# Kernel tuning notes

Hardware: AMD Instinct MI355X
Metric: run time of the kernel (lower is better)

The kernel has to match this reference:

```python
import jax, jax.numpy as jnp
import numpy as np

B, S, F, DK = 8, 2048, 1024, 128

def setup_inputs() -> dict:
    key = jax.random.key(0)
    ks = jax.random.split(key, 6)
    scale = 0.02
    return {
        "q": jax.random.normal(ks[0], (B, S, F), dtype=jnp.float32),
        "k": jax.random.normal(ks[1], (B, S, F), dtype=jnp.float32),
        "v": jax.random.normal(ks[2], (B, S, F), dtype=jnp.float32),
        "w_q": jax.random.normal(ks[3], (F, DK), dtype=jnp.float32) * scale,
        "w_k": jax.random.normal(ks[4], (F, DK), dtype=jnp.float32) * scale,
        "w_v": jax.random.normal(ks[5], (F, DK), dtype=jnp.float32) * scale,
    }

def reference(q, k, v, w_q, w_k, w_v):
    d_k = w_q.shape[-1]
    # bias-free linear projections: [B,S,F] @ [F,DK] -> [B,S,DK]
    qp = jnp.einsum("bsf,fd->bsd", q, w_q)
    kp = jnp.einsum("bsf,fd->bsd", k, w_k)
    vp = jnp.einsum("bsf,fd->bsd", v, w_v)
    # scaled dot-product scores: [B,S,S]
    scores = jnp.einsum("bqd,bkd->bqk", qp, kp) * (1.0 / jnp.sqrt(jnp.float32(d_k)))
    attn = jax.nn.softmax(scores, axis=-1)
    out = jnp.einsum("bqk,bkd->bqd", attn, vp)
    return out
```

## Files before the change

### kernel.cpp

```cpp
#include <hip/hip_runtime.h>
#include <hip/hip_bf16.h>

#define B_ 8
#define S_ 2048
#define F_ 1024
#define DK_ 128
#define M_ (B_*S_)

typedef unsigned short u16;
typedef short short8 __attribute__((ext_vector_type(8)));
typedef float f32x4 __attribute__((ext_vector_type(4)));
typedef float f32x16 __attribute__((ext_vector_type(16)));

__device__ __forceinline__ u16 f2bf(float f) {
    unsigned int u = __float_as_uint(f);
    u += 0x7FFFu + ((u >> 16) & 1u);
    return (u16)(u >> 16);
}
__device__ __forceinline__ unsigned int pack2(float a, float b) {
    return (unsigned int)f2bf(a) | ((unsigned int)f2bf(b) << 16);
}
__device__ __forceinline__ float fexp2(float x) {
#if __has_builtin(__builtin_amdgcn_exp2f)
    return __builtin_amdgcn_exp2f(x);
#else
    return exp2f(x);
#endif
}
__device__ __forceinline__ unsigned int cvt_pk_bf16(float lo, float hi) {
    unsigned int r;
    asm volatile("v_cvt_pk_bf16_f32 %0, %1, %2" : "=v"(r) : "v"(lo), "v"(hi));
    return r;
}

__global__ __launch_bounds__(256) void prep_wt(const float* __restrict__ wq,
                                               const float* __restrict__ wk,
                                               const float* __restrict__ wv,
                                               u16* __restrict__ WT) {
    int id = blockIdx.x * 256 + threadIdx.x;
    if (id >= 3 * DK_ * F_) return;
    int m   = id / (DK_ * F_);
    int rem = id - m * (DK_ * F_);
    int c   = rem / F_;
    int k   = rem - c * F_;
    const float* w = (m == 0) ? wq : (m == 1) ? wk : wv;
    float v = w[k * DK_ + c];
    if (m == 0) v *= 0.12751741951f;
    WT[id] = f2bf(v);
}

__global__ __launch_bounds__(256, 3) void proj(const float* __restrict__ xq,
                                               const float* __restrict__ xk,
                                               const float* __restrict__ xv,
                                               const u16* __restrict__ WT,
                                               u16* __restrict__ qp,
                                               u16* __restrict__ kp,
                                               u16* __restrict__ vpT) {
    const int mode = blockIdx.y;
    const float* X = (mode == 0) ? xq : (mode == 1) ? xk : xv;
    const u16*   W = WT + mode * (DK_ * F_);

    __shared__ u16 a_lds[64][40];
    __shared__ u16 w_lds[128][40];

    const int t    = threadIdx.x;
    const int lane = t & 63;
    const int wv_  = t >> 6;
    const int l15  = lane & 15, l4 = lane >> 4;
    const int row0 = blockIdx.x * 64;

    f32x4 acc[8];
#pragma unroll
    for (int j = 0; j < 8; ++j) acc[j] = f32x4{0.f, 0.f, 0.f, 0.f};

    for (int k0 = 0; k0 < F_; k0 += 32) {
        {
            int r = t >> 2, kk = (t & 3) * 8;
            const float4* src = (const float4*)(X + (size_t)(row0 + r) * F_ + k0 + kk);
            float4 f0 = src[0], f1 = src[1];
            int4 o0;
            o0.x = pack2(f0.x, f0.y); o0.y = pack2(f0.z, f0.w);
            o0.z = pack2(f1.x, f1.y); o0.w = pack2(f1.z, f1.w);
            *(int4*)&a_lds[r][kk] = o0;
        }
        {
            int c = t >> 1, kk = (t & 1) * 16;
            const int4* src = (const int4*)(W + (size_t)c * F_ + k0 + kk);
            *(int4*)&w_lds[c][kk]     = src[0];
            *(int4*)&w_lds[c][kk + 8] = src[1];
        }
        __syncthreads();

        short8 af = *(const short8*)&a_lds[wv_ * 16 + l15][l4 * 8];
        short8 bf[8];
#pragma unroll
        for (int ct = 0; ct < 8; ++ct)
            bf[ct] = *(const short8*)&w_lds[ct * 16 + l15][l4 * 8];

        if (mode < 2) {
#pragma unroll
            for (int ct = 0; ct < 8; ++ct)
                acc[ct] = __builtin_amdgcn_mfma_f32_16x16x32_bf16(af, bf[ct], acc[ct], 0, 0, 0);
        } else {
#pragma unroll
            for (int ct = 0; ct < 8; ++ct)
                acc[ct] = __builtin_amdgcn_mfma_f32_16x16x32_bf16(bf[ct], af, acc[ct], 0, 0, 0);
        }
        __syncthreads();
    }

    if (mode < 2) {
        u16* OUT = (mode == 0) ? qp : kp;
#pragma unroll
        for (int ct = 0; ct < 8; ++ct)
#pragma unroll
            for (int r = 0; r < 4; ++r) {
                int row = row0 + wv_ * 16 + l4 * 4 + r;
                int col = ct * 16 + l15;
                OUT[(size_t)row * DK_ + col] = f2bf(acc[ct][r]);
            }
    } else {
#pragma unroll
        for (int ct = 0; ct < 8; ++ct)
#pragma unroll
            for (int r = 0; r < 4; ++r) {
                int n = ct * 16 + l4 * 4 + r;
                int m = row0 + wv_ * 16 + l15;
                vpT[(size_t)n * M_ + m] = f2bf(acc[ct][r]);
            }
    }
}

union attn_lds_t {
    struct {
        __align__(16) unsigned char kbuf[2][16384];
        __align__(16) unsigned char vbuf[2][16384];
    } s;
    struct { float ob[64][132]; } e;
};

__global__ __launch_bounds__(512, 2) void attn(const u16* __restrict__ qp,
                                               const u16* __restrict__ kp,
                                               const u16* __restrict__ vpT,
                                               float* __restrict__ out) {
    __shared__ attn_lds_t u;
    __shared__ float m_lds[4][32], l_lds[4][32], gm_lds[2][32], gl_lds[2][32];

    const int t      = threadIdx.x;
    const int lane   = t & 63;
    const int wv_    = t >> 6;
    const int q_sub  = wv_ & 1;
    const int kv_sub = (wv_ >> 1) & 1;
    const int d_half = wv_ >> 2;
    const int r31    = lane & 31;
    const int hi     = lane >> 5;

    const int b  = blockIdx.x & 7;
    const int qi = blockIdx.x >> 3;
    const int qrow0 = b * S_ + qi * 64;
    const int kvb0  = b * S_;

    short8 qf[8];
#pragma unroll
    for (int c = 0; c < 8; ++c)
        qf[c] = *(const short8*)(qp + (size_t)(qrow0 + q_sub * 32 + r31) * DK_
                                    + c * 16 + hi * 8);

    f32x16 o4[2];
#pragma unroll
    for (int ct = 0; ct < 2; ++ct)
#pragma unroll
        for (int i = 0; i < 16; ++i) o4[ct][i] = 0.f;
    float mrun = -1.0e30f, lrun = 0.f;

    int4 gk0, gk1, gv0, gv1;
    const int f0 = t, f1 = 512 + t;
    const int kr0 = f0 >> 4, kc0 = f0 & 15, kr1 = f1 >> 4, kc1 = f1 & 15;
    const int vr0 = f0 >> 3, vc0 = f0 & 7,  vr1 = f1 >> 3, vc1 = f1 & 7;

#define LOADT(kvb)                                                               \
    {                                                                            \
        gk0 = *(const int4*)(kp + (size_t)((kvb) + kr0) * DK_ + kc0 * 8);        \
        gk1 = *(const int4*)(kp + (size_t)((kvb) + kr1) * DK_ + kc1 * 8);        \
        gv0 = *(const int4*)(vpT + (size_t)vr0 * M_ + (kvb) + vc0 * 8);          \
        gv1 = *(const int4*)(vpT + (size_t)vr1 * M_ + (kvb) + vc1 * 8);          \
    }
#define WRITET(nb)                                                               \
    {                                                                            \
        *(int4*)(u.s.kbuf[nb] + kr0 * 256 + ((kc0 ^ (kr0 & 15)) << 4)) = gk0;    \
        *(int4*)(u.s.kbuf[nb] + kr1 * 256 + ((kc1 ^ (kr1 & 15)) << 4)) = gk1;    \
        *(int4*)(u.s.vbuf[nb] + vr0 * 128 + ((vc0 ^ (vr0 & 7)) << 4)) = gv0;     \
        *(int4*)(u.s.vbuf[nb] + vr1 * 128 + ((vc1 ^ (vr1 & 7)) << 4)) = gv1;     \
    }

    LOADT(kvb0);
    WRITET(0);
    int cur = 0;

    for (int kt = 0; kt < 32; ++kt) {
        __syncthreads();

        if (kt < 31) LOADT(kvb0 + (kt + 1) * 64);

        const unsigned char* kb = u.s.kbuf[cur];
        const unsigned char* vb = u.s.vbuf[cur];

        const int krow  = kv_sub * 32 + r31;
        const int kbase = krow * 256;
        const int ksw   = krow & 15;
        short8 kf[8];
#pragma unroll
        for (int c = 0; c < 8; ++c)
            kf[c] = *(const short8*)(kb + kbase + (((c * 2 + hi) ^ ksw) << 4));

        f32x16 st;
#pragma unroll
        for (int i = 0; i < 16; ++i) st[i] = 0.f;
#pragma unroll
        for (int c = 0; c < 8; ++c)
            st = __builtin_amdgcn_mfma_f32_32x32x16_bf16(kf[c], qf[c], st, 0, 0, 0);

        float tm = st[0];
#pragma unroll
        for (int i = 1; i < 16; ++i) tm = fmaxf(tm, st[i]);
        tm = fmaxf(tm, __shfl_xor(tm, 32, 64));
        if (__any(tm > mrun + 8.0f)) {
            float mn = fmaxf(mrun, tm);
            float fs = fexp2(mrun - mn);
            mrun = mn;
            lrun *= fs;
#pragma unroll
            for (int ct = 0; ct < 2; ++ct)
#pragma unroll
                for (int i = 0; i < 16; ++i) o4[ct][i] *= fs;
        }
        float sum = 0.f;
#pragma unroll
        for (int i = 0; i < 16; ++i) { st[i] = fexp2(st[i] - mrun); sum += st[i]; }
        sum += __shfl_xor(sum, 32, 64);
        lrun += sum;

        short8 bp[2];
#pragma unroll
        for (int ch = 0; ch < 2; ++ch) {
            unsigned int wa = cvt_pk_bf16(st[ch * 8 + 0], st[ch * 8 + 1]);
            unsigned int wb = cvt_pk_bf16(st[ch * 8 + 2], st[ch * 8 + 3]);
            unsigned int wc = cvt_pk_bf16(st[ch * 8 + 4], st[ch * 8 + 5]);
            unsigned int wd = cvt_pk_bf16(st[ch * 8 + 6], st[ch * 8 + 7]);
            unsigned int xa = (unsigned int)__shfl_xor((int)wa, 32, 64);
            unsigned int xb = (unsigned int)__shfl_xor((int)wb, 32, 64);
            unsigned int xc = (unsigned int)__shfl_xor((int)wc, 32, 64);
            unsigned int xd = (unsigned int)__shfl_xor((int)wd, 32, 64);
            int4 w;
            w.x = (int)(hi ? xc : wa);
            w.y = (int)(hi ? xd : wb);
            w.z = (int)(hi ? wc : xa);
            w.w = (int)(hi ? wd : xb);
            bp[ch] = *(short8*)&w;
        }

        if (kt < 31) WRITET(cur ^ 1);

#pragma unroll
        for (int ct = 0; ct < 2; ++ct) {
            const int vrow  = d_half * 64 + ct * 32 + r31;
            const int vbase = vrow * 128;
            const int vsw   = vrow & 7;
#pragma unroll
            for (int ch = 0; ch < 2; ++ch) {
                short8 vf = *(const short8*)(vb + vbase
                                             + (((kv_sub * 4 + ch * 2 + hi) ^ vsw) << 4));
                o4[ct] = __builtin_amdgcn_mfma_f32_32x32x16_bf16(vf, bp[ch], o4[ct], 0, 0, 0);
            }
        }

        cur ^= 1;
    }
#undef LOADT
#undef WRITET

    __syncthreads();
    if (d_half == 0 && lane < 32) {
        m_lds[q_sub * 2 + kv_sub][r31] = mrun;
        l_lds[q_sub * 2 + kv_sub][r31] = lrun;
    }
    __syncthreads();
    if (t < 64) {
        int qs = t >> 5, qq = t & 31;
        float m0 = m_lds[qs * 2][qq], m1 = m_lds[qs * 2 + 1][qq];
        float gm = fmaxf(m0, m1);
        float gl = l_lds[qs * 2][qq] * fexp2(m0 - gm)
                 + l_lds[qs * 2 + 1][qq] * fexp2(m1 - gm);
        gm_lds[qs][qq] = gm;
        gl_lds[qs][qq] = gl;
    }
    __syncthreads();

    const float sc = fexp2(mrun - gm_lds[q_sub][r31]);
    const int qrow = q_sub * 32 + r31;
    if (kv_sub == 0) {
#pragma unroll
        for (int ct = 0; ct < 2; ++ct)
#pragma unroll
            for (int i = 0; i < 16; ++i) {
                int d = d_half * 64 + ct * 32 + (i & 3) + 8 * (i >> 2) + 4 * hi;
                u.e.ob[qrow][d] = o4[ct][i] * sc;
            }
    }
    __syncthreads();
    if (kv_sub == 1) {
#pragma unroll
        for (int ct = 0; ct < 2; ++ct)
#pragma unroll
            for (int i = 0; i < 16; ++i) {
                int d = d_half * 64 + ct * 32 + (i & 3) + 8 * (i >> 2) + 4 * hi;
                u.e.ob[qrow][d] += o4[ct][i] * sc;
            }
    }
    __syncthreads();

    {
        int row = t >> 3, d0 = (t & 7) * 16;
        float inv = 1.0f / gl_lds[row >> 5][row & 31];
        float* dst = out + (size_t)(qrow0 + row) * DK_ + d0;
#pragma unroll
        for (int j = 0; j < 16; j += 4) {
            float4 v;
            v.x = u.e.ob[row][d0 + j]     * inv;
            v.y = u.e.ob[row][d0 + j + 1] * inv;
            v.z = u.e.ob[row][d0 + j + 2] * inv;
            v.w = u.e.ob[row][d0 + j + 3] * inv;
            *(float4*)(dst + j) = v;
        }
    }
}

extern "C" void kernel_launch(void* const* d_in, const int* in_sizes, int n_in,
                              void* d_out, int out_size, void* d_ws, size_t ws_size,
                              hipStream_t stream) {
    const float* q  = (const float*)d_in[0];
    const float* k  = (const float*)d_in[1];
    const float* v  = (const float*)d_in[2];
    const float* wq = (const float*)d_in[3];
    const float* wk = (const float*)d_in[4];
    const float* wv = (const float*)d_in[5];
    float* out = (float*)d_out;

    char* ws = (char*)d_ws;
    u16* WT  = (u16*)ws;
    u16* qp  = (u16*)(ws + 786432);
    u16* kp  = (u16*)(ws + 786432 + 4194304);
    u16* vpT = (u16*)(ws + 786432 + 2 * 4194304);

    prep_wt<<<dim3(1536), dim3(256), 0, stream>>>(wq, wk, wv, WT);
    proj<<<dim3(256, 3), dim3(256), 0, stream>>>(q, k, v, WT, qp, kp, vpT);
    attn<<<dim3(256), dim3(512), 0, stream>>>(qp, kp, vpT, out);
}
```

Before: 83.50 us.

## Halve attention query tile to 32 rows and use permlane32 swap for P repack

The attention kernel now processes 32 query rows per block with 256 threads and launches 512 blocks instead of 256 blocks of 512 threads. The aim is to fill more CUs on the MI355X, at the cost of loading every K/V tile twice as often overall. It also splits the QK^T MFMA chain into two independent accumulators to shorten the dependency chain. The shuffle-plus-select repack of P is replaced with v_permlane32_swap, and the cross-half max and sum shuffles are deferred or folded into the final LDS reduction.

After: 85.88 us. 1.03x slower.

```diff
diff --git a/kernel.cpp b/kernel.cpp
--- a/kernel.cpp
+++ b/kernel.cpp
@@ -31,6 +31,9 @@
     unsigned int r;
     asm volatile("v_cvt_pk_bf16_f32 %0, %1, %2" : "=v"(r) : "v"(lo), "v"(hi));
     return r;
+}
+__device__ __forceinline__ void pl32_swap(unsigned int& a, unsigned int& b) {
+    asm volatile("v_permlane32_swap_b32 %0, %1" : "+v"(a), "+v"(b));
 }
 
 __global__ __launch_bounds__(256) void prep_wt(const float* __restrict__ wq,
@@ -136,35 +139,33 @@
         __align__(16) unsigned char kbuf[2][16384];
         __align__(16) unsigned char vbuf[2][16384];
     } s;
-    struct { float ob[64][132]; } e;
+    struct { float ob[32][132]; } e;
 };
 
-__global__ __launch_bounds__(512, 2) void attn(const u16* __restrict__ qp,
+__global__ __launch_bounds__(256, 2) void attn(const u16* __restrict__ qp,
                                                const u16* __restrict__ kp,
                                                const u16* __restrict__ vpT,
                                                float* __restrict__ out) {
     __shared__ attn_lds_t u;
-    __shared__ float m_lds[4][32], l_lds[4][32], gm_lds[2][32], gl_lds[2][32];
+    __shared__ float m_lds[2][32], l_lds[2][2][32], gm_lds[32], gl_lds[32];
 
     const int t      = threadIdx.x;
     const int lane   = t & 63;
     const int wv_    = t >> 6;
-    const int q_sub  = wv_ & 1;
-    const int kv_sub = (wv_ >> 1) & 1;
-    const int d_half = wv_ >> 2;
+    const int kv_sub = wv_ & 1;
+    const int d_half = wv_ >> 1;
     const int r31    = lane & 31;
     const int hi     = lane >> 5;
 
     const int b  = blockIdx.x & 7;
     const int qi = blockIdx.x >> 3;
-    const int qrow0 = b * S_ + qi * 64;
+    const int qrow0 = b * S_ + qi * 32;
     const int kvb0  = b * S_;
 
     short8 qf[8];
 #pragma unroll
     for (int c = 0; c < 8; ++c)
-        qf[c] = *(const short8*)(qp + (size_t)(qrow0 + q_sub * 32 + r31) * DK_
-                                    + c * 16 + hi * 8);
+        qf[c] = *(const short8*)(qp + (size_t)(qrow0 + r31) * DK_ + c * 16 + hi * 8);
 
     f32x16 o4[2];
 #pragma unroll
@@ -173,24 +174,30 @@
         for (int i = 0; i < 16; ++i) o4[ct][i] = 0.f;
     float mrun = -1.0e30f, lrun = 0.f;
 
-    int4 gk0, gk1, gv0, gv1;
-    const int f0 = t, f1 = 512 + t;
-    const int kr0 = f0 >> 4, kc0 = f0 & 15, kr1 = f1 >> 4, kc1 = f1 & 15;
-    const int vr0 = f0 >> 3, vc0 = f0 & 7,  vr1 = f1 >> 3, vc1 = f1 & 7;
-
-#define LOADT(kvb)                                                               \
-    {                                                                            \
-        gk0 = *(const int4*)(kp + (size_t)((kvb) + kr0) * DK_ + kc0 * 8);        \
-        gk1 = *(const int4*)(kp + (size_t)((kvb) + kr1) * DK_ + kc1 * 8);        \
-        gv0 = *(const int4*)(vpT + (size_t)vr0 * M_ + (kvb) + vc0 * 8);          \
-        gv1 = *(const int4*)(vpT + (size_t)vr1 * M_ + (kvb) + vc1 * 8);          \
-    }
-#define WRITET(nb)                                                               \
-    {                                                                            \
-        *(int4*)(u.s.kbuf[nb] + kr0 * 256 + ((kc0 ^ (kr0 & 15)) << 4)) = gk0;    \
-        *(int4*)(u.s.kbuf[nb] + kr1 * 256 + ((kc1 ^ (kr1 & 15)) << 4)) = gk1;    \
-        *(int4*)(u.s.vbuf[nb] + vr0 * 128 + ((vc0 ^ (vr0 & 7)) << 4)) = gv0;     \
-        *(int4*)(u.s.vbuf[nb] + vr1 * 128 + ((vc1 ^ (vr1 & 7)) << 4)) = gv1;     \
+    int4 gk[4], gv[4];
+    int kr[4], kc[4], vr[4], vc[4];
+#pragma unroll
+    for (int j = 0; j < 4; ++j) {
+        int f = t + 256 * j;
+        kr[j] = f >> 4; kc[j] = f & 15;
+        vr[j] = f >> 3; vc[j] = f & 7;
+    }
+
+#define LOADT(kvb)                                                                \
+    {                                                                             \
+        _Pragma("unroll")                                                         \
+        for (int j = 0; j < 4; ++j) {                                             \
+            gk[j] = *(const int4*)(kp + (size_t)((kvb) + kr[j]) * DK_ + kc[j] * 8);\
+            gv[j] = *(const int4*)(vpT + (size_t)vr[j] * M_ + (kvb) + vc[j] * 8); \
+        }                                                                         \
+    }
+#define WRITET(nb)                                                                \
+    {                                                                             \
+        _Pragma("unroll")                                                         \
+        for (int j = 0; j < 4; ++j) {                                             \
+            *(int4*)(u.s.kbuf[nb] + kr[j] * 256 + ((kc[j] ^ (kr[j] & 15)) << 4)) = gk[j]; \
+            *(int4*)(u.s.vbuf[nb] + vr[j] * 128 + ((vc[j] ^ (vr[j] & 7)) << 4)) = gv[j];  \
+        }                                                                         \
     }
 
     LOADT(kvb0);
@@ -213,18 +220,23 @@
         for (int c = 0; c < 8; ++c)
             kf[c] = *(const short8*)(kb + kbase + (((c * 2 + hi) ^ ksw) << 4));
 
+        f32x16 sa, sb;
+#pragma unroll
+        for (int i = 0; i < 16; ++i) { sa[i] = 0.f; sb[i] = 0.f; }
+#pragma unroll
+        for (int c = 0; c < 4; ++c) {
+            sa = __builtin_amdgcn_mfma_f32_32x32x16_bf16(kf[c],     qf[c],     sa, 0, 0, 0);
+            sb = __builtin_amdgcn_mfma_f32_32x32x16_bf16(kf[c + 4], qf[c + 4], sb, 0, 0, 0);
+        }
         f32x16 st;
 #pragma unroll
-        for (int i = 0; i < 16; ++i) st[i] = 0.f;
-#pragma unroll
-        for (int c = 0; c < 8; ++c)
-            st = __builtin_amdgcn_mfma_f32_32x32x16_bf16(kf[c], qf[c], st, 0, 0, 0);
+        for (int i = 0; i < 16; ++i) st[i] = sa[i] + sb[i];
 
         float tm = st[0];
 #pragma unroll
         for (int i = 1; i < 16; ++i) tm = fmaxf(tm, st[i]);
-        tm = fmaxf(tm, __shfl_xor(tm, 32, 64));
         if (__any(tm > mrun + 8.0f)) {
+            tm = fmaxf(tm, __shfl_xor(tm, 32, 64));
             float mn = fmaxf(mrun, tm);
             float fs = fexp2(mrun - mn);
             mrun = mn;
@@ -234,28 +246,26 @@
 #pragma unroll
                 for (int i = 0; i < 16; ++i) o4[ct][i] *= fs;
         }
-        float sum = 0.f;
-#pragma unroll
-        for (int i = 0; i < 16; ++i) { st[i] = fexp2(st[i] - mrun); sum += st[i]; }
-        sum += __shfl_xor(sum, 32, 64);
-        lrun += sum;
+        float s0 = 0.f, s1 = 0.f;
+#pragma unroll
+        for (int i = 0; i < 16; i += 2) {
+            st[i]     = fexp2(st[i] - mrun);
+            st[i + 1] = fexp2(st[i + 1] - mrun);
+            s0 += st[i]; s1 += st[i + 1];
+        }
+        lrun += s0 + s1;
 
         short8 bp[2];
 #pragma unroll
         for (int ch = 0; ch < 2; ++ch) {
-            unsigned int wa = cvt_pk_bf16(st[ch * 8 + 0], st[ch * 8 + 1]);
-            unsigned int wb = cvt_pk_bf16(st[ch * 8 + 2], st[ch * 8 + 3]);
-            unsigned int wc = cvt_pk_bf16(st[ch * 8 + 4], st[ch * 8 + 5]);
-            unsigned int wd = cvt_pk_bf16(st[ch * 8 + 6], st[ch * 8 + 7]);
-            unsigned int xa = (unsigned int)__shfl_xor((int)wa, 32, 64);
-            unsigned int xb = (unsigned int)__shfl_xor((int)wb, 32, 64);
-            unsigned int xc = (unsigned int)__shfl_xor((int)wc, 32, 64);
-            unsigned int xd = (unsigned int)__shfl_xor((int)wd, 32, 64);
+            unsigned int A1 = cvt_pk_bf16(st[ch * 8 + 0], st[ch * 8 + 1]);
+            unsigned int A2 = cvt_pk_bf16(st[ch * 8 + 2], st[ch * 8 + 3]);
+            unsigned int A3 = cvt_pk_bf16(st[ch * 8 + 4], st[ch * 8 + 5]);
+            unsigned int A4 = cvt_pk_bf16(st[ch * 8 + 6], st[ch * 8 + 7]);
+            pl32_swap(A1, A3);
+            pl32_swap(A2, A4);
             int4 w;
-            w.x = (int)(hi ? xc : wa);
-            w.y = (int)(hi ? xd : wb);
-            w.z = (int)(hi ? wc : xa);
-            w.w = (int)(hi ? wd : xb);
+            w.x = (int)A1; w.y = (int)A2; w.z = (int)A3; w.w = (int)A4;
             bp[ch] = *(short8*)&w;
         }
 
@@ -280,31 +290,29 @@
 #undef WRITET
 
     __syncthreads();
-    if (d_half == 0 && lane < 32) {
-        m_lds[q_sub * 2 + kv_sub][r31] = mrun;
-        l_lds[q_sub * 2 + kv_sub][r31] = lrun;
-    }
-    __syncthreads();
-    if (t < 64) {
-        int qs = t >> 5, qq = t & 31;
-        float m0 = m_lds[qs * 2][qq], m1 = m_lds[qs * 2 + 1][qq];
+    if (d_half == 0) {
+        l_lds[kv_sub][hi][r31] = lrun;
+        if (lane < 32) m_lds[kv_sub][r31] = mrun;
+    }
+    __syncthreads();
+    if (t < 32) {
+        float m0 = m_lds[0][t], m1 = m_lds[1][t];
         float gm = fmaxf(m0, m1);
-        float gl = l_lds[qs * 2][qq] * fexp2(m0 - gm)
-                 + l_lds[qs * 2 + 1][qq] * fexp2(m1 - gm);
-        gm_lds[qs][qq] = gm;
-        gl_lds[qs][qq] = gl;
-    }
-    __syncthreads();
-
-    const float sc = fexp2(mrun - gm_lds[q_sub][r31]);
-    const int qrow = q_sub * 32 + r31;
+        float gl = (l_lds[0][0][t] + l_lds[0][1][t]) * fexp2(m0 - gm)
+                 + (l_lds[1][0][t] + l_lds[1][1][t]) * fexp2(m1 - gm);
+        gm_lds[t] = gm;
+        gl_lds[t] = gl;
+    }
+    __syncthreads();
+
+    const float sc = fexp2(mrun - gm_lds[r31]);
     if (kv_sub == 0) {
 #pragma unroll
         for (int ct = 0; ct < 2; ++ct)
 #pragma unroll
             for (int i = 0; i < 16; ++i) {
                 int d = d_half * 64 + ct * 32 + (i & 3) + 8 * (i >> 2) + 4 * hi;
-                u.e.ob[qrow][d] = o4[ct][i] * sc;
+                u.e.ob[r31][d] = o4[ct][i] * sc;
             }
     }
     __syncthreads();
@@ -314,14 +322,14 @@
 #pragma unroll
             for (int i = 0; i < 16; ++i) {
                 int d = d_half * 64 + ct * 32 + (i & 3) + 8 * (i >> 2) + 4 * hi;
-                u.e.ob[qrow][d] += o4[ct][i] * sc;
+                u.e.ob[r31][d] += o4[ct][i] * sc;
             }
     }
     __syncthreads();
 
     {
         int row = t >> 3, d0 = (t & 7) * 16;
-        float inv = 1.0f / gl_lds[row >> 5][row & 31];
+        float inv = 1.0f / gl_lds[row];
         float* dst = out + (size_t)(qrow0 + row) * DK_ + d0;
 #pragma unroll
         for (int j = 0; j < 16; j += 4) {
@@ -354,5 +362,5 @@
 
     prep_wt<<<dim3(1536), dim3(256), 0, stream>>>(wq, wk, wv, WT);
     proj<<<dim3(256, 3), dim3(256), 0, stream>>>(q, k, v, WT, qp, kp, vpT);
-    attn<<<dim3(256), dim3(512), 0, stream>>>(qp, kp, vpT, out);
-}
+    attn<<<dim3(512), dim3(256), 0, stream>>>(qp, kp, vpT, out);
+}
```
